# Optimization experiments

Measured on AMD Instinct MI355X. Metric: run time of the kernel, lower is better.

Reference implementation:

```python
import jax, jax.numpy as jnp
import numpy as np

N_Q = 16384; N_S = 16384; NN = 32; F_IN = 128; F_OUT = 256
K = 15; DIM = 3
RADIUS = 10.0
KP_EXTENT_CFG = 1.0      # config.NETWORK.KP_EXTENT (also scales learned offsets)
DENSITY = 5.0            # config.NETWORK.DENSITY_PARAMETER
EXTENT = KP_EXTENT_CFG * RADIUS / DENSITY   # 2.0
K_RADIUS = 1.5 * EXTENT
OFFSET_DIM = DIM * (K - 1)  # modulated=False, version=0 -> 42


def setup_inputs() -> dict:
    key = jax.random.key(0)
    ks = jax.random.split(key, 8)
    query_points = jax.random.uniform(ks[0], (N_Q, DIM), dtype=jnp.float32)
    support_points = jax.random.uniform(ks[1], (N_S, DIM), dtype=jnp.float32)
    neighbors = jax.random.randint(ks[2], (N_Q, NN), 0, N_S)
    features = jax.random.normal(ks[3], (N_S, F_IN), dtype=jnp.float32)
    # kernel points: fixed disposition inside ball of radius 1.5*extent, first point at center
    kp = jax.random.normal(ks[4], (K, DIM), dtype=jnp.float32)
    kp = kp / jnp.linalg.norm(kp, axis=1, keepdims=True) * (0.7 * K_RADIUS)
    K_points = kp.at[0].set(0.0)
    weight = jax.random.normal(ks[5], (K, F_IN, F_OUT), dtype=jnp.float32) / np.sqrt(F_IN)
    deformable_weight = jax.random.normal(ks[6], (K, F_IN, OFFSET_DIM), dtype=jnp.float32) / np.sqrt(F_IN)
    bias = jnp.zeros((OFFSET_DIM,), dtype=jnp.float32)
    return {"query_points": query_points, "support_points": support_points,
            "neighbors": neighbors, "features": features, "K_points": K_points,
            "weight": weight, "deformable_weight": deformable_weight, "bias": bias}


def _gather_neighb(query_points, support_points, neighbors, features):
    # pad with shadow point (far away) and zero feature row, as in KPConv_ops
    sp = jnp.concatenate([support_points, jnp.full((1, DIM), 1e6, support_points.dtype)], 0)
    ft = jnp.concatenate([features, jnp.zeros((1, features.shape[1]), features.dtype)], 0)
    rel = sp[neighbors] - query_points[:, None, :]   # [n, nn, 3]
    nfeat = ft[neighbors]                            # [n, nn, f]
    return rel, nfeat


def _linear_influence(sq_dist):
    # KP_INFLUENCE='linear': relu(1 - d/extent); CONVOLUTION_MODE='sum'
    return jnp.maximum(1.0 - jnp.sqrt(sq_dist) / EXTENT, 0.0)


def reference(query_points, support_points, neighbors, features, K_points,
              weight, deformable_weight, bias):
    rel, nfeat = _gather_neighb(query_points, support_points, neighbors, features)

    # --- rigid KPConv producing offsets (version=0) ---
    d0 = rel[:, :, None, :] - K_points[None, None, :, :]   # [n, nn, K, 3]
    sq0 = jnp.sum(d0 * d0, axis=-1)                        # [n, nn, K]
    w0 = _linear_influence(sq0)
    wf0 = jnp.einsum('enk,enf->ekf', w0, nfeat)            # [n, K, f]
    feat0 = jnp.einsum('ekf,kfo->eo', wf0, deformable_weight) + bias  # [n, 42]

    # not modulated: reshape to offsets, prepend zero offset for center kernel point
    offsets = feat0.reshape(-1, K - 1, DIM)
    offsets = jnp.concatenate([jnp.zeros_like(offsets[:, :1, :]), offsets], axis=1)
    offsets = offsets * KP_EXTENT_CFG                      # [n, K, 3]

    # --- deformable KPConv ---
    def_kp = K_points[None, :, :] + offsets                # [n, K, 3]
    d1 = rel[:, :, None, :] - def_kp[:, None, :, :]        # [n, nn, K, 3]
    sq1 = jnp.sum(d1 * d1, axis=-1)                        # [n, nn, K]
    w1 = _linear_influence(sq1)                            # out-of-range neighbors get 0 weight
    wf1 = jnp.einsum('enk,enf->ekf', w1, nfeat)            # [n, K, f]
    out = jnp.einsum('ekf,kfo->eo', wf1, weight)           # [n, f_out]
    return out
```

## Files before the change

### kernel.cpp

```cpp
#include <hip/hip_runtime.h>
#include <hip/hip_bf16.h>
#include <math.h>

typedef __attribute__((ext_vector_type(8))) short bf16x8;
typedef __attribute__((ext_vector_type(4))) float f32x4;

#define NQ 16384
#define NN 32
#define FI 128
#define FO 256
#define KPN 15
#define OD 42
#define INV_EXT 0.5f

#define WS_FP1    0u
#define WS_FP2    (8u * 1024u * 1024u)
#define WS_BSW    (12u * 1024u * 1024u)
#define WS_DWBH   (13u * 1024u * 1024u)
#define WS_DWBL   (WS_DWBH + 196608u)

static __device__ __forceinline__ unsigned short f2bf(float x) {
    union { __hip_bfloat16 h; unsigned short u; } cv;
    cv.h = __float2bfloat16(x);
    return cv.u;
}
static __device__ __forceinline__ float bf2f(unsigned short h) {
    union { unsigned int u; float f; } cv;
    cv.u = ((unsigned int)h) << 16;
    return cv.f;
}

union U8 { unsigned short u[8]; bf16x8 v; };

__global__ void pre_all(const float* __restrict__ feat,
                        unsigned int* __restrict__ fp1, unsigned int* __restrict__ fp2,
                        const float* __restrict__ w, unsigned short* __restrict__ Bsw,
                        const float* __restrict__ dw,
                        unsigned short* __restrict__ dhi, unsigned short* __restrict__ dlo)
{
    const int b = blockIdx.x, t = threadIdx.x;
    if (b < 4096) {
        const int tid = b * 256 + t;
        const int s = tid >> 6, r = tid & 63;
        const int fp = r >> 4, low = r & 15;
        const float a = feat[s * FI + fp * 32 + low];
        const float c = feat[s * FI + fp * 32 + 16 + low];
        const unsigned short ha = f2bf(a), hc = f2bf(c);
        const unsigned int w0 = (unsigned int)ha | ((unsigned int)hc << 16);
        const unsigned int w1 = (unsigned int)f2bf(a - bf2f(ha)) |
                                ((unsigned int)f2bf(c - bf2f(hc)) << 16);
        uint2 pr; pr.x = w0; pr.y = w1;
        *(uint2*)&fp1[s * 128 + fp * 32 + low * 2] = pr;
        fp2[s * 64 + fp * 16 + low] = w0;
    } else if (b < 4096 + 256) {
        const int tid = (b - 4096) * 256 + t;
        const int lane = tid & 63;
        const int kt   = (tid >> 6) & 63;
        const int nt   = tid >> 12;
        const int n    = nt * 16 + (lane & 15);
        const int kbase = kt * 32 + (lane >> 4) * 8;
        unsigned int p[4];
        #pragma unroll
        for (int jj = 0; jj < 4; jj++) {
            unsigned int lo, hi;
            {
                const int kk = kbase + 2 * jj;
                const int f = kk >> 4, k = kk & 15;
                lo = (k < KPN) ? f2bf(w[(k * FI + f) * FO + n]) : 0u;
            }
            {
                const int kk = kbase + 2 * jj + 1;
                const int f = kk >> 4, k = kk & 15;
                hi = (k < KPN) ? f2bf(w[(k * FI + f) * FO + n]) : 0u;
            }
            p[jj] = lo | (hi << 16);
        }
        unsigned int* op = (unsigned int*)&Bsw[tid * 8];
        op[0] = p[0]; op[1] = p[1]; op[2] = p[2]; op[3] = p[3];
    } else {
        const int tid = (b - 4352) * 256 + t;
        const int lane = tid & 63;
        const int kt   = (tid >> 6) & 63;
        const int nt   = tid >> 12;
        const int o    = nt * 16 + (lane & 15);
        const int kbase = kt * 32 + (lane >> 4) * 8;
        #pragma unroll
        for (int j = 0; j < 8; j++) {
            const int kf = kbase + j;
            const int f = kf >> 4, k = kf & 15;
            float v = (k < KPN && o < OD) ? dw[(k * FI + f) * OD + o] : 0.f;
            unsigned short h = f2bf(v);
            dhi[tid * 8 + j] = h;
            dlo[tid * 8 + j] = f2bf(v - bf2f(h));
        }
    }
}

__global__ __launch_bounds__(512, 4)
void k_fused(const float* __restrict__ query, const float* __restrict__ support,
             const int* __restrict__ neighbors, const unsigned int* __restrict__ fp1,
             const unsigned int* __restrict__ fp2, const float* __restrict__ kpoints,
             const unsigned short* __restrict__ dwB_hi,
             const unsigned short* __restrict__ dwB_lo,
             const unsigned short* __restrict__ Bsw,
             const float* __restrict__ bias, float* __restrict__ out)
{
    __shared__ unsigned short wf_hi[16384];
    __shared__ unsigned short wf_lo[16384];
    __shared__ float relx[1024], rely[1024], relz[1024];
    __shared__ unsigned short nbr_s[1024];
    __shared__ float kp_s[48];

    const int t = threadIdx.x;
    const int qbase = blockIdx.x * 32;
    if (t < 45) kp_s[t] = kpoints[t];
    if (t >= 45 && t < 48) kp_s[t] = 0.f;

    #pragma unroll
    for (int ii = 0; ii < 2; ii++) {
        const int i = ii * 512 + t;
        const int e = i >> 5, n = i & 31;
        const int q = qbase + e;
        const int idx = neighbors[q * NN + n];
        nbr_s[i] = (unsigned short)idx;
        relx[i] = support[idx * 3 + 0] - query[q * 3 + 0];
        rely[i] = support[idx * 3 + 1] - query[q * 3 + 1];
        relz[i] = support[idx * 3 + 2] - query[q * 3 + 2];
    }
    __syncthreads();

    const int wave = t >> 6, lane = t & 63;
    const int quad = lane >> 4, low = lane & 15;
    const int kb = (low < KPN) ? low * 3 : 0;

    U8 ah[4], al[4];
    {
        const float kx = kp_s[kb + 0], ky = kp_s[kb + 1], kz = kp_s[kb + 2];
        #pragma unroll
        for (int ei = 0; ei < 4; ei++) {
            const int ee = wave * 4 + ei;
            #pragma unroll
            for (int j = 0; j < 8; j++) {
                const int ni = ee * 32 + quad * 8 + j;
                const float dx = relx[ni] - kx;
                const float dy = rely[ni] - ky;
                const float dz = relz[ni] - kz;
                const float d = sqrtf(dx * dx + dy * dy + dz * dz);
                float w = 1.0f - d * INV_EXT;
                w = (low < KPN && w > 0.f) ? w : 0.f;
                const unsigned short h = f2bf(w);
                ah[ei].u[j] = h;
                al[ei].u[j] = f2bf(w - bf2f(h));
            }
        }
    }

    f32x4 acc = {0.f, 0.f, 0.f, 0.f};
    const int et = (wave >= 3) ? 1 : 0;
    const int nt = wave - et * 3;

    for (int c = 0; c < 4; c++) {
        #pragma unroll 2
        for (int ei = 0; ei < 4; ei++) {
            const int ee = wave * 4 + ei;
            union { unsigned int u[4]; bf16x8 v; } bhA, blA, bhB, blB;
            #pragma unroll
            for (int jj = 0; jj < 4; jj++) {
                const int r0 = nbr_s[ee * 32 + quad * 8 + 2 * jj];
                const int r1 = nbr_s[ee * 32 + quad * 8 + 2 * jj + 1];
                const uint2 d0 = *(const uint2*)&fp1[r0 * 128 + c * 32 + low * 2];
                const uint2 d1 = *(const uint2*)&fp1[r1 * 128 + c * 32 + low * 2];
                bhA.u[jj] = __builtin_amdgcn_perm(d1.x, d0.x, 0x05040100u);
                bhB.u[jj] = __builtin_amdgcn_perm(d1.x, d0.x, 0x07060302u);
                blA.u[jj] = __builtin_amdgcn_perm(d1.y, d0.y, 0x05040100u);
                blB.u[jj] = __builtin_amdgcn_perm(d1.y, d0.y, 0x07060302u);
            }
            #pragma unroll
            for (int hh2 = 0; hh2 < 2; hh2++) {
                const bf16x8 bh = hh2 ? bhB.v : bhA.v;
                const bf16x8 bl = hh2 ? blB.v : blA.v;
                f32x4 o = {0.f, 0.f, 0.f, 0.f};
                o = __builtin_amdgcn_mfma_f32_16x16x32_bf16(al[ei].v, bh, o, 0, 0, 0);
                o = __builtin_amdgcn_mfma_f32_16x16x32_bf16(ah[ei].v, bl, o, 0, 0, 0);
                o = __builtin_amdgcn_mfma_f32_16x16x32_bf16(ah[ei].v, bh, o, 0, 0, 0);
                const int fc   = hh2 * 16 + low;
                const int cblk = fc + (quad >> 1) * 32;
                const int slot = ee ^ fc;
                const int hw   = cblk * 256 + slot * 8 + (quad & 1) * 4;
                const unsigned short h0 = f2bf(o[0]), h1 = f2bf(o[1]);
                const unsigned short h2 = f2bf(o[2]), h3 = f2bf(o[3]);
                uint2 ph;
                ph.x = (unsigned int)h0 | ((unsigned int)h1 << 16);
                ph.y = (unsigned int)h2 | ((unsigned int)h3 << 16);
                *(uint2*)&wf_hi[hw] = ph;
                uint2 pl;
                pl.x = (unsigned int)f2bf(o[0] - bf2f(h0)) |
                       ((unsigned int)f2bf(o[1] - bf2f(h1)) << 16);
                pl.y = (unsigned int)f2bf(o[2] - bf2f(h2)) |
                       ((unsigned int)f2bf(o[3] - bf2f(h3)) << 16);
                *(uint2*)&wf_lo[hw] = pl;
            }
        }
        __syncthreads();
        if (wave < 6) {
            const bf16x8* Bh = (const bf16x8*)dwB_hi;
            const bf16x8* Bl = (const bf16x8*)dwB_lo;
            #pragma unroll 4
            for (int ktl = 0; ktl < 16; ktl++) {
                const int fcq  = ktl * 2 + (quad >> 1);
                const int cblk = fcq + (quad & 1) * 32;
                const int slot = (et * 16 + low) ^ fcq;
                bf16x8 a_h = *(const bf16x8*)&wf_hi[cblk * 256 + slot * 8];
                bf16x8 a_l = *(const bf16x8*)&wf_lo[cblk * 256 + slot * 8];
                const int ktg = c * 16 + ktl;
                bf16x8 b_h = Bh[(nt * 64 + ktg) * 64 + lane];
                bf16x8 b_l = Bl[(nt * 64 + ktg) * 64 + lane];
                acc = __builtin_amdgcn_mfma_f32_16x16x32_bf16(a_l, b_h, acc, 0, 0, 0);
                acc = __builtin_amdgcn_mfma_f32_16x16x32_bf16(a_h, b_l, acc, 0, 0, 0);
                acc = __builtin_amdgcn_mfma_f32_16x16x32_bf16(a_h, b_h, acc, 0, 0, 0);
            }
        }
        __syncthreads();
    }

    float* dk_s = (float*)wf_lo;
    if (wave < 6) {
        const int o = nt * 16 + low;
        if (o < OD) {
            const float bo = bias[o] + kp_s[3 + o];
            #pragma unroll
            for (int r = 0; r < 4; r++) {
                const int ee = et * 16 + quad * 4 + r;
                dk_s[ee * 48 + 3 + o] = bo + acc[r];
            }
        }
    } else {
        const int idx2 = (wave - 6) * 64 + lane;
        if (idx2 < 96) dk_s[(idx2 / 3) * 48 + (idx2 % 3)] = kp_s[idx2 % 3];
    }
    __syncthreads();

    U8 af[4];
    #pragma unroll
    for (int ei = 0; ei < 4; ei++) {
        const int ee = wave * 4 + ei;
        const float kx = dk_s[ee * 48 + kb + 0];
        const float ky = dk_s[ee * 48 + kb + 1];
        const float kz = dk_s[ee * 48 + kb + 2];
        #pragma unroll
        for (int j = 0; j < 8; j++) {
            const int ni = ee * 32 + quad * 8 + j;
            const float dx = relx[ni] - kx;
            const float dy = rely[ni] - ky;
            const float dz = relz[ni] - kz;
            const float d = sqrtf(dx * dx + dy * dy + dz * dz);
            float w = 1.0f - d * INV_EXT;
            w = (low < KPN && w > 0.f) ? w : 0.f;
            af[ei].u[j] = f2bf(w);
        }
    }

    f32x4 acc00 = {0,0,0,0}, acc01 = {0,0,0,0};
    f32x4 acc10 = {0,0,0,0}, acc11 = {0,0,0,0};
    const int nt0 = wave * 2, nt1 = nt0 + 1;
    const bf16x8* Bp = (const bf16x8*)Bsw;

    for (int c = 0; c < 4; c++) {
        #pragma unroll
        for (int ei = 0; ei < 4; ei++) {
            const int ee = wave * 4 + ei;
            union { unsigned int u[4]; bf16x8 v; } bA, bB;
            #pragma unroll
            for (int jj = 0; jj < 4; jj++) {
                const int r0 = nbr_s[ee * 32 + quad * 8 + 2 * jj];
                const int r1 = nbr_s[ee * 32 + quad * 8 + 2 * jj + 1];
                const unsigned int d0 = fp2[r0 * 64 + c * 16 + low];
                const unsigned int d1 = fp2[r1 * 64 + c * 16 + low];
                bA.u[jj] = __builtin_amdgcn_perm(d1, d0, 0x05040100u);
                bB.u[jj] = __builtin_amdgcn_perm(d1, d0, 0x07060302u);
            }
            #pragma unroll
            for (int hh2 = 0; hh2 < 2; hh2++) {
                const bf16x8 b = hh2 ? bB.v : bA.v;
                f32x4 o = {0.f, 0.f, 0.f, 0.f};
                o = __builtin_amdgcn_mfma_f32_16x16x32_bf16(af[ei].v, b, o, 0, 0, 0);
                const int fc   = hh2 * 16 + low;
                const int cblk = fc + (quad >> 1) * 32;
                const int slot = ee ^ fc;
                const int hw   = cblk * 256 + slot * 8 + (quad & 1) * 4;
                uint2 ph;
                ph.x = (unsigned int)f2bf(o[0]) | ((unsigned int)f2bf(o[1]) << 16);
                ph.y = (unsigned int)f2bf(o[2]) | ((unsigned int)f2bf(o[3]) << 16);
                *(uint2*)&wf_hi[hw] = ph;
            }
        }
        __syncthreads();
        #pragma unroll 4
        for (int ktl = 0; ktl < 16; ktl++) {
            const int fcq  = ktl * 2 + (quad >> 1);
            const int cblk = fcq + (quad & 1) * 32;
            const int s0 = (low ^ fcq) * 8;
            const int s1 = ((16 + low) ^ fcq) * 8;
            bf16x8 a0 = *(const bf16x8*)&wf_hi[cblk * 256 + s0];
            bf16x8 a1 = *(const bf16x8*)&wf_hi[cblk * 256 + s1];
            const int ktg = c * 16 + ktl;
            bf16x8 b0 = Bp[(nt0 * 64 + ktg) * 64 + lane];
            bf16x8 b1 = Bp[(nt1 * 64 + ktg) * 64 + lane];
            acc00 = __builtin_amdgcn_mfma_f32_16x16x32_bf16(a0, b0, acc00, 0, 0, 0);
            acc01 = __builtin_amdgcn_mfma_f32_16x16x32_bf16(a0, b1, acc01, 0, 0, 0);
            acc10 = __builtin_amdgcn_mfma_f32_16x16x32_bf16(a1, b0, acc10, 0, 0, 0);
            acc11 = __builtin_amdgcn_mfma_f32_16x16x32_bf16(a1, b1, acc11, 0, 0, 0);
        }
        __syncthreads();
    }

    #pragma unroll
    for (int r = 0; r < 4; r++) {
        const int e0 = quad * 4 + r;
        out[(qbase + e0) * FO + nt0 * 16 + low] = acc00[r];
        out[(qbase + e0) * FO + nt1 * 16 + low] = acc01[r];
        out[(qbase + 16 + e0) * FO + nt0 * 16 + low] = acc10[r];
        out[(qbase + 16 + e0) * FO + nt1 * 16 + low] = acc11[r];
    }
}

extern "C" void kernel_launch(void* const* d_in, const int* in_sizes, int n_in,
                              void* d_out, int out_size, void* d_ws, size_t ws_size,
                              hipStream_t stream) {
    const float* query     = (const float*)d_in[0];
    const float* support   = (const float*)d_in[1];
    const int*   neighbors = (const int*)  d_in[2];
    const float* features  = (const float*)d_in[3];
    const float* kpoints   = (const float*)d_in[4];
    const float* weight    = (const float*)d_in[5];
    const float* dweight   = (const float*)d_in[6];
    const float* bias      = (const float*)d_in[7];
    float*       out       = (float*)d_out;

    char* ws = (char*)d_ws;
    unsigned int*   fp1  = (unsigned int*)(ws + WS_FP1);
    unsigned int*   fp2  = (unsigned int*)(ws + WS_FP2);
    unsigned short* Bsw  = (unsigned short*)(ws + WS_BSW);
    unsigned short* dwBh = (unsigned short*)(ws + WS_DWBH);
    unsigned short* dwBl = (unsigned short*)(ws + WS_DWBL);

    pre_all<<<4400, 256, 0, stream>>>(features, fp1, fp2, weight, Bsw,
                                      dweight, dwBh, dwBl);
    k_fused<<<NQ / 32, 512, 0, stream>>>(query, support, neighbors, fp1, fp2,
                                         kpoints, dwBh, dwBl, Bsw, bias, out);
}
```

Baseline: 178.6 us.

## Shrink shared memory by halving offset-stage chunks and vectorize feature packing

The offset-producing stage now processes 16-feature chunks over 8 iterations instead of 32-feature chunks over 4. This lets the hi and lo weighted-feature buffers share one 32 KB LDS array, and the deformed kernel-point table gets its own small array. The aim is to cut LDS use so more blocks fit per CU, with launch bounds raised to 6 accordingly. The feature packing pre-kernel is also vectorized with float4 loads and uint4 stores. In exchange the fp1 layout changes to interleaved hi/lo per element, and the offset stage runs more barrier rounds.

Result: slower. 249.2 us (+39.6%).

```diff
diff --git a/kernel.cpp b/kernel.cpp
--- a/kernel.cpp
+++ b/kernel.cpp
@@ -39,21 +39,34 @@
                         unsigned short* __restrict__ dhi, unsigned short* __restrict__ dlo)
 {
     const int b = blockIdx.x, t = threadIdx.x;
-    if (b < 4096) {
-        const int tid = b * 256 + t;
-        const int s = tid >> 6, r = tid & 63;
-        const int fp = r >> 4, low = r & 15;
-        const float a = feat[s * FI + fp * 32 + low];
-        const float c = feat[s * FI + fp * 32 + 16 + low];
-        const unsigned short ha = f2bf(a), hc = f2bf(c);
-        const unsigned int w0 = (unsigned int)ha | ((unsigned int)hc << 16);
-        const unsigned int w1 = (unsigned int)f2bf(a - bf2f(ha)) |
-                                ((unsigned int)f2bf(c - bf2f(hc)) << 16);
-        uint2 pr; pr.x = w0; pr.y = w1;
-        *(uint2*)&fp1[s * 128 + fp * 32 + low * 2] = pr;
-        fp2[s * 64 + fp * 16 + low] = w0;
-    } else if (b < 4096 + 256) {
-        const int tid = (b - 4096) * 256 + t;
+    if (b < 1024) {
+        const int g  = b * 256 + t;
+        const int lq = g & 3;
+        const int fp = (g >> 2) & 3;
+        const int s  = g >> 4;
+        const float4* f4 = (const float4*)feat;
+        const float4 A = f4[s * 32 + fp * 8 + lq];
+        const float4 C = f4[s * 32 + fp * 8 + 4 + lq];
+        const float av[4] = {A.x, A.y, A.z, A.w};
+        const float cv[4] = {C.x, C.y, C.z, C.w};
+        uint4 p1a, p1c, p2;
+        unsigned int* pa = (unsigned int*)&p1a;
+        unsigned int* pc = (unsigned int*)&p1c;
+        unsigned int* p2p = (unsigned int*)&p2;
+        #pragma unroll
+        for (int e = 0; e < 4; e++) {
+            const unsigned short ha = f2bf(av[e]), hc = f2bf(cv[e]);
+            const unsigned short la = f2bf(av[e] - bf2f(ha));
+            const unsigned short lc = f2bf(cv[e] - bf2f(hc));
+            pa[e]  = (unsigned int)ha | ((unsigned int)la << 16);
+            pc[e]  = (unsigned int)hc | ((unsigned int)lc << 16);
+            p2p[e] = (unsigned int)ha | ((unsigned int)hc << 16);
+        }
+        *(uint4*)&fp1[s * 128 + fp * 32 + lq * 4]      = p1a;
+        *(uint4*)&fp1[s * 128 + fp * 32 + 16 + lq * 4] = p1c;
+        *(uint4*)&fp2[s * 64 + fp * 16 + lq * 4]       = p2;
+    } else if (b < 1024 + 256) {
+        const int tid = (b - 1024) * 256 + t;
         const int lane = tid & 63;
         const int kt   = (tid >> 6) & 63;
         const int nt   = tid >> 12;
@@ -78,7 +91,7 @@
         unsigned int* op = (unsigned int*)&Bsw[tid * 8];
         op[0] = p[0]; op[1] = p[1]; op[2] = p[2]; op[3] = p[3];
     } else {
-        const int tid = (b - 4352) * 256 + t;
+        const int tid = (b - 1280) * 256 + t;
         const int lane = tid & 63;
         const int kt   = (tid >> 6) & 63;
         const int nt   = tid >> 12;
@@ -96,7 +109,7 @@
     }
 }
 
-__global__ __launch_bounds__(512, 4)
+__global__ __launch_bounds__(512, 6)
 void k_fused(const float* __restrict__ query, const float* __restrict__ support,
              const int* __restrict__ neighbors, const unsigned int* __restrict__ fp1,
              const unsigned int* __restrict__ fp2, const float* __restrict__ kpoints,
@@ -105,9 +118,9 @@
              const unsigned short* __restrict__ Bsw,
              const float* __restrict__ bias, float* __restrict__ out)
 {
-    __shared__ unsigned short wf_hi[16384];
-    __shared__ unsigned short wf_lo[16384];
+    __shared__ unsigned short wf[16384];
     __shared__ float relx[1024], rely[1024], relz[1024];
+    __shared__ float dk_s[32 * 45];
     __shared__ unsigned short nbr_s[1024];
     __shared__ float kp_s[48];
 
@@ -159,71 +172,66 @@
     const int et = (wave >= 3) ? 1 : 0;
     const int nt = wave - et * 3;
 
-    for (int c = 0; c < 4; c++) {
+    for (int c2 = 0; c2 < 8; c2++) {
         #pragma unroll 2
         for (int ei = 0; ei < 4; ei++) {
             const int ee = wave * 4 + ei;
-            union { unsigned int u[4]; bf16x8 v; } bhA, blA, bhB, blB;
+            union { unsigned int u[4]; bf16x8 v; } bh, bl;
             #pragma unroll
             for (int jj = 0; jj < 4; jj++) {
                 const int r0 = nbr_s[ee * 32 + quad * 8 + 2 * jj];
                 const int r1 = nbr_s[ee * 32 + quad * 8 + 2 * jj + 1];
-                const uint2 d0 = *(const uint2*)&fp1[r0 * 128 + c * 32 + low * 2];
-                const uint2 d1 = *(const uint2*)&fp1[r1 * 128 + c * 32 + low * 2];
-                bhA.u[jj] = __builtin_amdgcn_perm(d1.x, d0.x, 0x05040100u);
-                bhB.u[jj] = __builtin_amdgcn_perm(d1.x, d0.x, 0x07060302u);
-                blA.u[jj] = __builtin_amdgcn_perm(d1.y, d0.y, 0x05040100u);
-                blB.u[jj] = __builtin_amdgcn_perm(d1.y, d0.y, 0x07060302u);
-            }
-            #pragma unroll
-            for (int hh2 = 0; hh2 < 2; hh2++) {
-                const bf16x8 bh = hh2 ? bhB.v : bhA.v;
-                const bf16x8 bl = hh2 ? blB.v : blA.v;
-                f32x4 o = {0.f, 0.f, 0.f, 0.f};
-                o = __builtin_amdgcn_mfma_f32_16x16x32_bf16(al[ei].v, bh, o, 0, 0, 0);
-                o = __builtin_amdgcn_mfma_f32_16x16x32_bf16(ah[ei].v, bl, o, 0, 0, 0);
-                o = __builtin_amdgcn_mfma_f32_16x16x32_bf16(ah[ei].v, bh, o, 0, 0, 0);
-                const int fc   = hh2 * 16 + low;
-                const int cblk = fc + (quad >> 1) * 32;
-                const int slot = ee ^ fc;
-                const int hw   = cblk * 256 + slot * 8 + (quad & 1) * 4;
-                const unsigned short h0 = f2bf(o[0]), h1 = f2bf(o[1]);
-                const unsigned short h2 = f2bf(o[2]), h3 = f2bf(o[3]);
-                uint2 ph;
-                ph.x = (unsigned int)h0 | ((unsigned int)h1 << 16);
-                ph.y = (unsigned int)h2 | ((unsigned int)h3 << 16);
-                *(uint2*)&wf_hi[hw] = ph;
-                uint2 pl;
-                pl.x = (unsigned int)f2bf(o[0] - bf2f(h0)) |
-                       ((unsigned int)f2bf(o[1] - bf2f(h1)) << 16);
-                pl.y = (unsigned int)f2bf(o[2] - bf2f(h2)) |
-                       ((unsigned int)f2bf(o[3] - bf2f(h3)) << 16);
-                *(uint2*)&wf_lo[hw] = pl;
-            }
+                const unsigned int g0 = fp1[r0 * 128 + c2 * 16 + low];
+                const unsigned int g1 = fp1[r1 * 128 + c2 * 16 + low];
+                bh.u[jj] = __builtin_amdgcn_perm(g1, g0, 0x05040100u);
+                bl.u[jj] = __builtin_amdgcn_perm(g1, g0, 0x07060302u);
+            }
+            f32x4 o = {0.f, 0.f, 0.f, 0.f};
+            o = __builtin_amdgcn_mfma_f32_16x16x32_bf16(al[ei].v, bh.v, o, 0, 0, 0);
+            o = __builtin_amdgcn_mfma_f32_16x16x32_bf16(ah[ei].v, bl.v, o, 0, 0, 0);
+            o = __builtin_amdgcn_mfma_f32_16x16x32_bf16(ah[ei].v, bh.v, o, 0, 0, 0);
+            const int cblk = low + (quad >> 1) * 16;
+            const int slot = ee ^ low;
+            const int hw   = cblk * 256 + slot * 8 + (quad & 1) * 4;
+            const unsigned short h0 = f2bf(o[0]), h1 = f2bf(o[1]);
+            const unsigned short h2 = f2bf(o[2]), h3 = f2bf(o[3]);
+            uint2 ph;
+            ph.x = (unsigned int)h0 | ((unsigned int)h1 << 16);
+            ph.y = (unsigned int)h2 | ((unsigned int)h3 << 16);
+            *(uint2*)&wf[hw] = ph;
+            uint2 pl;
+            pl.x = (unsigned int)f2bf(o[0] - bf2f(h0)) |
+                   ((unsigned int)f2bf(o[1] - bf2f(h1)) << 16);
+            pl.y = (unsigned int)f2bf(o[2] - bf2f(h2)) |
+                   ((unsigned int)f2bf(o[3] - bf2f(h3)) << 16);
+            *(uint2*)&wf[8192 + hw] = pl;
         }
         __syncthreads();
         if (wave < 6) {
             const bf16x8* Bh = (const bf16x8*)dwB_hi;
             const bf16x8* Bl = (const bf16x8*)dwB_lo;
             #pragma unroll 4
-            for (int ktl = 0; ktl < 16; ktl++) {
-                const int fcq  = ktl * 2 + (quad >> 1);
-                const int cblk = fcq + (quad & 1) * 32;
-                const int slot = (et * 16 + low) ^ fcq;
-                bf16x8 a_h = *(const bf16x8*)&wf_hi[cblk * 256 + slot * 8];
-                bf16x8 a_l = *(const bf16x8*)&wf_lo[cblk * 256 + slot * 8];
-                const int ktg = c * 16 + ktl;
+            for (int ktl = 0; ktl < 8; ktl++) {
+                const int fl   = ktl * 2 + (quad >> 1);
+                const int cblk = fl + (quad & 1) * 16;
+                const int slot = (et * 16 + low) ^ fl;
+                const int hw   = cblk * 256 + slot * 8;
+                bf16x8 a_h = *(const bf16x8*)&wf[hw];
+                bf16x8 a_l = *(const bf16x8*)&wf[8192 + hw];
+                const int ktg = c2 * 8 + ktl;
                 bf16x8 b_h = Bh[(nt * 64 + ktg) * 64 + lane];
                 bf16x8 b_l = Bl[(nt * 64 + ktg) * 64 + lane];
                 acc = __builtin_amdgcn_mfma_f32_16x16x32_bf16(a_l, b_h, acc, 0, 0, 0);
                 acc = __builtin_amdgcn_mfma_f32_16x16x32_bf16(a_h, b_l, acc, 0, 0, 0);
                 acc = __builtin_amdgcn_mfma_f32_16x16x32_bf16(a_h, b_h, acc, 0, 0, 0);
             }
+        } else if (c2 == 0) {
+            const int idx2 = (wave - 6) * 64 + lane;
+            if (idx2 < 96) dk_s[(idx2 / 3) * 45 + (idx2 % 3)] = kp_s[idx2 % 3];
         }
         __syncthreads();
     }
 
-    float* dk_s = (float*)wf_lo;
     if (wave < 6) {
         const int o = nt * 16 + low;
         if (o < OD) {
@@ -231,12 +239,9 @@
             #pragma unroll
             for (int r = 0; r < 4; r++) {
                 const int ee = et * 16 + quad * 4 + r;
-                dk_s[ee * 48 + 3 + o] = bo + acc[r];
-            }
-        }
-    } else {
-        const int idx2 = (wave - 6) * 64 + lane;
-        if (idx2 < 96) dk_s[(idx2 / 3) * 48 + (idx2 % 3)] = kp_s[idx2 % 3];
+                dk_s[ee * 45 + 3 + o] = bo + acc[r];
+            }
+        }
     }
     __syncthreads();
 
@@ -244,9 +249,9 @@
     #pragma unroll
     for (int ei = 0; ei < 4; ei++) {
         const int ee = wave * 4 + ei;
-        const float kx = dk_s[ee * 48 + kb + 0];
-        const float ky = dk_s[ee * 48 + kb + 1];
-        const float kz = dk_s[ee * 48 + kb + 2];
+        const float kx = dk_s[ee * 45 + kb + 0];
+        const float ky = dk_s[ee * 45 + kb + 1];
+        const float kz = dk_s[ee * 45 + kb + 2];
         #pragma unroll
         for (int j = 0; j < 8; j++) {
             const int ni = ee * 32 + quad * 8 + j;
@@ -291,7 +296,7 @@
                 uint2 ph;
                 ph.x = (unsigned int)f2bf(o[0]) | ((unsigned int)f2bf(o[1]) << 16);
                 ph.y = (unsigned int)f2bf(o[2]) | ((unsigned int)f2bf(o[3]) << 16);
-                *(uint2*)&wf_hi[hw] = ph;
+                *(uint2*)&wf[hw] = ph;
             }
         }
         __syncthreads();
@@ -301,8 +306,8 @@
             const int cblk = fcq + (quad & 1) * 32;
             const int s0 = (low ^ fcq) * 8;
             const int s1 = ((16 + low) ^ fcq) * 8;
-            bf16x8 a0 = *(const bf16x8*)&wf_hi[cblk * 256 + s0];
-            bf16x8 a1 = *(const bf16x8*)&wf_hi[cblk * 256 + s1];
+            bf16x8 a0 = *(const bf16x8*)&wf[cblk * 256 + s0];
+            bf16x8 a1 = *(const bf16x8*)&wf[cblk * 256 + s1];
             const int ktg = c * 16 + ktl;
             bf16x8 b0 = Bp[(nt0 * 64 + ktg) * 64 + lane];
             bf16x8 b1 = Bp[(nt1 * 64 + ktg) * 64 + lane];
@@ -344,7 +349,7 @@
     unsigned short* dwBh = (unsigned short*)(ws + WS_DWBH);
     unsigned short* dwBl = (unsigned short*)(ws + WS_DWBL);
 
-    pre_all<<<4400, 256, 0, stream>>>(features, fp1, fp2, weight, Bsw,
+    pre_all<<<1328, 256, 0, stream>>>(features, fp1, fp2, weight, Bsw,
                                       dweight, dwBh, dwBl);
     k_fused<<<NQ / 32, 512, 0, stream>>>(query, support, neighbors, fp1, fp2,
                                          kpoints, dwBh, dwBl, Bsw, bias, out);
```
